# Performance work log

Measured on AMD Instinct MI355X. Metric: run time of the kernel, lower is better.

The kernel has to match this reference:

```python
import jax, jax.numpy as jnp
import numpy as np

B, T, C = 2, 4096, 768
H = 12
D = C // H  # head_size = 64


def setup_inputs() -> dict:
    key = jax.random.key(0)
    k1, k2, k3 = jax.random.split(key, 3)
    x = jax.random.normal(k1, (B, T, C), dtype=jnp.float32)
    w_attn = jax.random.normal(k2, (C, 3 * C), dtype=jnp.float32) * (C ** -0.5)
    b_attn = jnp.zeros((3 * C,), dtype=jnp.float32)
    w_proj = jax.random.normal(k3, (C, C), dtype=jnp.float32) * (C ** -0.5)
    b_proj = jnp.zeros((C,), dtype=jnp.float32)
    return {"x": x, "w_attn": w_attn, "b_attn": b_attn, "w_proj": w_proj, "b_proj": b_proj}


def reference(x, w_attn, b_attn, w_proj, b_proj):
    Bx, Tx, Cx = x.shape
    # fused QKV projection
    qkv = x @ w_attn + b_attn  # (B, T, 3C)
    q, k, v = jnp.split(qkv, 3, axis=2)
    # (B, H, T, D)
    q = q.reshape(Bx, Tx, H, D).transpose(0, 2, 1, 3)
    k = k.reshape(Bx, Tx, H, D).transpose(0, 2, 1, 3)
    v = v.reshape(Bx, Tx, H, D).transpose(0, 2, 1, 3)
    scale = 1.0 / jnp.sqrt(jnp.asarray(D, dtype=x.dtype))
    scores = jnp.einsum('bhqd,bhkd->bhqk', q, k) * scale  # (B, H, T, T)
    causal = jnp.tril(jnp.ones((Tx, Tx), dtype=bool))
    scores = jnp.where(causal, scores, jnp.asarray(-jnp.inf, dtype=scores.dtype))
    attn = jax.nn.softmax(scores, axis=-1)
    y = jnp.einsum('bhqk,bhkd->bhqd', attn, v)  # (B, H, T, D)
    y = y.transpose(0, 2, 1, 3).reshape(Bx, Tx, Cx)
    return y @ w_proj + b_proj
```

## Files before the change

kernel.cpp:

```cpp
#include <hip/hip_runtime.h>
#include <stdint.h>

#define B_   2
#define T_   4096
#define C_   768
#define H_   12
#define D_   64
#define BH_  24
#define M_   8192
#define K_   768
#define N1_  2304

#define NEG_BIG (-1.0e30f)
#define QSCALE 0.18033688011112042f

typedef short bf16x8 __attribute__((ext_vector_type(8)));
typedef float f32x4  __attribute__((ext_vector_type(4)));
typedef float f32x16 __attribute__((ext_vector_type(16)));
typedef uint32_t u32x4 __attribute__((ext_vector_type(4)));
typedef int i32x2 __attribute__((ext_vector_type(2)));

typedef const __attribute__((address_space(1))) void* as1cv;
typedef __attribute__((address_space(3))) void*       as3v;

__device__ __forceinline__ void gload_lds16(const void* g, void* l) {
  __builtin_amdgcn_global_load_lds((as1cv)g, (as3v)l, 16, 0, 0);
}

__device__ __forceinline__ unsigned short f2bf(float f) {
  uint32_t x = __builtin_bit_cast(uint32_t, f);
  uint32_t r = (x + 0x7fffu + ((x >> 16) & 1u)) >> 16;
  return (unsigned short)r;
}

__device__ __forceinline__ unsigned short f2bf_hu(float f) {
  return (unsigned short)((__builtin_bit_cast(uint32_t, f) + 0x8000u) >> 16);
}

#if __has_builtin(__builtin_amdgcn_perm)
__device__ __forceinline__ uint32_t pack_hu(float lo, float hi) {
  uint32_t a = __builtin_bit_cast(uint32_t, lo) + 0x8000u;
  uint32_t b = __builtin_bit_cast(uint32_t, hi) + 0x8000u;
  return __builtin_amdgcn_perm(b, a, 0x07060302u);
}
#else
__device__ __forceinline__ uint32_t pack_hu(float lo, float hi) {
  uint32_t a = __builtin_bit_cast(uint32_t, lo) + 0x8000u;
  uint32_t b = __builtin_bit_cast(uint32_t, hi) + 0x8000u;
  return (b & 0xFFFF0000u) | (a >> 16);
}
#endif

__device__ __forceinline__ float bfu(uint32_t w, int hb) {
  return __builtin_bit_cast(float, hb ? (w & 0xFFFF0000u) : (w << 16));
}

#if __has_builtin(__builtin_amdgcn_permlane32_swap)
#define HAVE_PLSWAP 1
#else
#define HAVE_PLSWAP 0
#endif

#if __has_builtin(__builtin_amdgcn_exp2f)
__device__ __forceinline__ float fast_exp2(float x) { return __builtin_amdgcn_exp2f(x); }
#else
__device__ __forceinline__ float fast_exp2(float x) { return __expf(x * 0.69314718056f); }
#endif

__global__ void cast_kernel(const float* __restrict__ in, unsigned short* __restrict__ out, int n4) {
  int idx = blockIdx.x * blockDim.x + threadIdx.x;
  int stride = gridDim.x * blockDim.x;
  for (int i = idx; i < n4; i += stride) {
    float4 v = reinterpret_cast<const float4*>(in)[i];
    ushort4 o;
    o.x = f2bf(v.x); o.y = f2bf(v.y); o.z = f2bf(v.z); o.w = f2bf(v.w);
    reinterpret_cast<ushort4*>(out)[i] = o;
  }
}

__global__ void transpose_cast2(const float* __restrict__ a, unsigned short* __restrict__ oa,
                                const float* __restrict__ b, unsigned short* __restrict__ ob) {
  __shared__ float tile[32][33];
  const int bx = blockIdx.x;
  const float* in; unsigned short* out; int N, cb;
  if (bx < 72) { in = a; out = oa; N = 2304; cb = bx; }
  else         { in = b; out = ob; N = 768;  cb = bx - 72; }
  const int tx = threadIdx.x, ty = threadIdx.y;
  const int n = cb * 32 + tx;
  #pragma unroll
  for (int r = 0; r < 4; ++r) {
    int k = blockIdx.y * 32 + ty + r * 8;
    tile[ty + r * 8][tx] = in[(size_t)k * N + n];
  }
  __syncthreads();
  const int k = blockIdx.y * 32 + tx;
  #pragma unroll
  for (int r = 0; r < 4; ++r) {
    int nn = cb * 32 + ty + r * 8;
    out[(size_t)nn * K_ + k] = f2bf(tile[tx][ty + r * 8]);
  }
}

template <int MODE>
__global__ __launch_bounds__(256) void gemm_kernel(
    const unsigned short* __restrict__ A, const unsigned short* __restrict__ BT,
    const float* __restrict__ bias,
    unsigned short* __restrict__ o0, unsigned short* __restrict__ o1,
    unsigned short* __restrict__ o2, float* __restrict__ fo) {
  __shared__ __align__(16) unsigned short Al[128 * 32];
  __shared__ __align__(16) unsigned short Bl[128 * 32];
  const int tid = threadIdx.x;
  const int w = tid >> 6, lane = tid & 63;
  const int g = lane >> 4, c16 = lane & 15;
  const int wr = w >> 1, wc = w & 1;
  const int m0 = blockIdx.x * 128, n0 = blockIdx.y * 128;

  f32x4 acc[4][4] = {};

  for (int k0 = 0; k0 < K_; k0 += 32) {
    __syncthreads();
    #pragma unroll
    for (int q = 0; q < 2; ++q) {
      const int ch = (w * 2 + q) * 64 + lane;
      const int row = ch >> 2, kb = ch & 3;
      gload_lds16(A  + (size_t)(m0 + row) * K_ + k0 + kb * 8, &Al[(w * 2 + q) * 512]);
      gload_lds16(BT + (size_t)(n0 + row) * K_ + k0 + kb * 8, &Bl[(w * 2 + q) * 512]);
    }
    __syncthreads();
    bf16x8 af[4], bfr[4];
    #pragma unroll
    for (int i = 0; i < 4; ++i) {
      af[i]  = *reinterpret_cast<const bf16x8*>(&Al[(wr * 64 + i * 16 + c16) * 32 + g * 8]);
      bfr[i] = *reinterpret_cast<const bf16x8*>(&Bl[(wc * 64 + i * 16 + c16) * 32 + g * 8]);
    }
    #pragma unroll
    for (int i = 0; i < 4; ++i)
      #pragma unroll
      for (int j = 0; j < 4; ++j)
        acc[i][j] = __builtin_amdgcn_mfma_f32_16x16x32_bf16(af[i], bfr[j], acc[i][j], 0, 0, 0);
  }

  const int which = (MODE == 0) ? (n0 / 768) : 0;
  #pragma unroll
  for (int i = 0; i < 4; ++i) {
    const int mbase = m0 + wr * 64 + i * 16 + g * 4;
    const int bb2 = mbase >> 12, tb = mbase & 4095;
    #pragma unroll
    for (int j2 = 0; j2 < 4; ++j2) {
      const int n = n0 + wc * 64 + j2 * 16 + c16;
      const float bv = bias[n];
      if constexpr (MODE == 0) {
        const int cc = n - which * 768;
        const int hh2 = cc >> 6, dd = cc & 63;
        const size_t hb = ((size_t)bb2 * H_ + hh2) * T_ * D_;
        if (which == 0) {
          const int addr0 = tb * 64 + dd;
          #pragma unroll
          for (int j = 0; j < 4; ++j)
            o0[hb + addr0 + j * 64] = f2bf_hu((acc[i][j2][j] + bv) * QSCALE);
        } else if (which == 1) {
          const int addr0 = ((tb >> 5) * 4 + (dd >> 4)) * 512 +
                            ((tb & 31) + ((dd >> 3) & 1) * 32) * 8 + (dd & 7);
          #pragma unroll
          for (int j = 0; j < 4; ++j)
            o1[hb + addr0 + j * 8] = f2bf_hu(acc[i][j2][j] + bv);
        } else {
          const int addr0 = (tb >> 6) * 4096 + (dd >> 5) * 2048 +
                            ((tb >> 4) & 3) * 512 +
                            ((dd & 31) + ((tb >> 3) & 1) * 32) * 8 + (tb & 7);
          #pragma unroll
          for (int j = 0; j < 4; ++j)
            o2[hb + addr0 + j] = f2bf_hu(acc[i][j2][j] + bv);
        }
      } else {
        #pragma unroll
        for (int j = 0; j < 4; ++j)
          fo[(size_t)(mbase + j) * 768 + n] = acc[i][j2][j] + bv;
      }
    }
  }
}

__global__ __launch_bounds__(256, 2) void attn_kernel(
    const unsigned short* __restrict__ Qb, const unsigned short* __restrict__ Kb,
    const unsigned short* __restrict__ Vt, unsigned short* __restrict__ Yb) {
  __shared__ float Ml[3][2][64];
  __shared__ float Ll[3][2][64];
  __shared__ uint32_t Ylp[3][32][64];

  const int tidx = threadIdx.x;
  const int wv = tidx >> 6;
  const int lane = tidx & 63;
  const int q31 = lane & 31, hi = lane >> 5;
  const int bid = blockIdx.x;
  const int bh = bid % BH_;
  const int strip = (T_ / 64 - 1) - bid / BH_;
  const int q0 = strip * 64;
  const int qgA = q0 + q31;
  const int qgB = q0 + 32 + q31;

  const int bb = bh / H_, hh = bh % H_;
  const size_t hoff = (size_t)bh * T_ * D_;
  const unsigned short* Qh = Qb + hoff;
  const unsigned short* Kh = Kb + hoff + lane * 8;
  const unsigned short* Vh = Vt + hoff + lane * 8;

  bf16x8 qfA[4], qfB[4];
  #pragma unroll
  for (int s = 0; s < 4; ++s) {
    qfA[s] = *reinterpret_cast<const bf16x8*>(&Qh[(size_t)qgA * D_ + s * 16 + hi * 8]);
    qfB[s] = *reinterpret_cast<const bf16x8*>(&Qh[(size_t)qgB * D_ + s * 16 + hi * 8]);
  }

  float mA = NEG_BIG, lA = 0.f, mB = NEG_BIG, lB = 0.f;
  f32x16 yA0 = {}, yA1 = {}, yB0 = {}, yB1 = {};

  const int nt = strip + 1;

  bf16x8 kf[8];
  {
    const unsigned short* kT = Kh + wv * 4096;
    #pragma unroll
    for (int s = 0; s < 8; ++s)
      kf[s] = *reinterpret_cast<const bf16x8*>(kT + (s >> 2) * 2048 + (s & 3) * 512);
  }

  for (int it = wv; it < nt; it += 4) {
    const int kv0 = it << 6;

    const unsigned short* vT = Vh + it * 4096;
    bf16x8 vlo[4], vhi[4];
    #pragma unroll
    for (int ks = 0; ks < 4; ++ks) {
      vlo[ks] = *reinterpret_cast<const bf16x8*>(vT + ks * 512);
      vhi[ks] = *reinterpret_cast<const bf16x8*>(vT + 2048 + ks * 512);
    }

    f32x16 sA0 = {}, sA1 = {}, sB0 = {}, sB1 = {};
    #pragma unroll
    for (int s = 0; s < 4; ++s) {
      sA0 = __builtin_amdgcn_mfma_f32_32x32x16_bf16(kf[s], qfA[s], sA0, 0, 0, 0);
      sB0 = __builtin_amdgcn_mfma_f32_32x32x16_bf16(kf[s], qfB[s], sB0, 0, 0, 0);
    }
    #pragma unroll
    for (int s = 0; s < 4; ++s) {
      sA1 = __builtin_amdgcn_mfma_f32_32x32x16_bf16(kf[4 + s], qfA[s], sA1, 0, 0, 0);
      sB1 = __builtin_amdgcn_mfma_f32_32x32x16_bf16(kf[4 + s], qfB[s], sB1, 0, 0, 0);
    }

    {
      const unsigned short* kT = Kh + (it + 4) * 4096;
      #pragma unroll
      for (int s = 0; s < 8; ++s)
        kf[s] = *reinterpret_cast<const bf16x8*>(kT + (s >> 2) * 2048 + (s & 3) * 512);
    }

    if (it == strip) {
      #pragma unroll
      for (int r = 0; r < 16; ++r) {
        const int kvl = (r & 3) + 8 * (r >> 2) + 4 * hi;
        sA0[r] = (kv0 + kvl > qgA)      ? NEG_BIG : sA0[r];
        sA1[r] = NEG_BIG;
        sB1[r] = (kv0 + 32 + kvl > qgB) ? NEG_BIG : sB1[r];
      }
    }

    {
      float a[16];
      #pragma unroll
      for (int r = 0; r < 8; ++r) a[r] = fmaxf(sA0[2 * r], sA0[2 * r + 1]);
      #pragma unroll
      for (int r = 0; r < 8; ++r) a[8 + r] = fmaxf(sA1[2 * r], sA1[2 * r + 1]);
      #pragma unroll
      for (int st = 8; st > 0; st >>= 1)
        #pragma unroll
        for (int r = 0; r < 16; ++r) if (r < st) a[r] = fmaxf(a[r], a[r + st]);
      float tmax = a[0];
      tmax = fmaxf(tmax, __shfl_xor(tmax, 32));

      if (__any(tmax > mA + 11.5f)) {
        const float mnew = fmaxf(mA, tmax);
        const float alpha = fast_exp2(mA - mnew);
        mA = mnew;
        lA *= alpha;
        #pragma unroll
        for (int r = 0; r < 16; ++r) { yA0[r] *= alpha; yA1[r] *= alpha; }
      }
      #pragma unroll
      for (int r = 0; r < 16; ++r) {
        sA0[r] = fast_exp2(sA0[r] - mA);
        sA1[r] = fast_exp2(sA1[r] - mA);
      }
      #pragma unroll
      for (int r = 0; r < 8; ++r) a[r] = sA0[2 * r] + sA0[2 * r + 1];
      #pragma unroll
      for (int r = 0; r < 8; ++r) a[8 + r] = sA1[2 * r] + sA1[2 * r + 1];
      #pragma unroll
      for (int st = 8; st > 0; st >>= 1)
        #pragma unroll
        for (int r = 0; r < 16; ++r) if (r < st) a[r] = a[r] + a[r + st];
      float rsum = a[0];
      rsum += __shfl_xor(rsum, 32);
      lA += rsum;

      bf16x8 pf[4];
#if HAVE_PLSWAP
#define MK_PF(KS, SH, GA, HA)                                                 \
      {                                                                       \
        uint32_t g0 = pack_hu(SH[(GA)*4 + 0], SH[(GA)*4 + 1]);                \
        uint32_t g1 = pack_hu(SH[(GA)*4 + 2], SH[(GA)*4 + 3]);                \
        uint32_t h0 = pack_hu(SH[(HA)*4 + 0], SH[(HA)*4 + 1]);                \
        uint32_t h1 = pack_hu(SH[(HA)*4 + 2], SH[(HA)*4 + 3]);                \
        i32x2 r0 = __builtin_amdgcn_permlane32_swap((int)g0, (int)h0, false, false); \
        i32x2 r1 = __builtin_amdgcn_permlane32_swap((int)g1, (int)h1, false, false); \
        u32x4 t;                                                              \
        t[0] = (uint32_t)r0[0];                                               \
        t[1] = (uint32_t)r1[0];                                               \
        t[2] = (uint32_t)r0[1];                                               \
        t[3] = (uint32_t)r1[1];                                               \
        pf[KS] = __builtin_bit_cast(bf16x8, t);                               \
      }
#else
#define MK_PF(KS, SH, GA, HA)                                                 \
      {                                                                       \
        uint32_t g0 = pack_hu(SH[(GA)*4 + 0], SH[(GA)*4 + 1]);                \
        uint32_t g1 = pack_hu(SH[(GA)*4 + 2], SH[(GA)*4 + 3]);                \
        uint32_t h0 = pack_hu(SH[(HA)*4 + 0], SH[(HA)*4 + 1]);                \
        uint32_t h1 = pack_hu(SH[(HA)*4 + 2], SH[(HA)*4 + 3]);                \
        uint32_t sg0 = (uint32_t)__shfl_xor((int)g0, 32);                     \
        uint32_t sg1 = (uint32_t)__shfl_xor((int)g1, 32);                     \
        uint32_t sh0 = (uint32_t)__shfl_xor((int)h0, 32);                     \
        uint32_t sh1 = (uint32_t)__shfl_xor((int)h1, 32);                     \
        u32x4 t;                                                              \
        t[0] = hi ? sh0 : g0;                                                 \
        t[1] = hi ? sh1 : g1;                                                 \
        t[2] = hi ? h0 : sg0;                                                 \
        t[3] = hi ? h1 : sg1;                                                 \
        pf[KS] = __builtin_bit_cast(bf16x8, t);                               \
      }
#endif
      MK_PF(0, sA0, 0, 1)
      MK_PF(1, sA0, 2, 3)
      MK_PF(2, sA1, 0, 1)
      MK_PF(3, sA1, 2, 3)

      #pragma unroll
      for (int ks = 0; ks < 4; ++ks)
        yA0 = __builtin_amdgcn_mfma_f32_32x32x16_bf16(vlo[ks], pf[ks], yA0, 0, 0, 0);
      #pragma unroll
      for (int ks = 0; ks < 4; ++ks)
        yA1 = __builtin_amdgcn_mfma_f32_32x32x16_bf16(vhi[ks], pf[ks], yA1, 0, 0, 0);
    }

    {
      float a[16];
      #pragma unroll
      for (int r = 0; r < 8; ++r) a[r] = fmaxf(sB0[2 * r], sB0[2 * r + 1]);
      #pragma unroll
      for (int r = 0; r < 8; ++r) a[8 + r] = fmaxf(sB1[2 * r], sB1[2 * r + 1]);
      #pragma unroll
      for (int st = 8; st > 0; st >>= 1)
        #pragma unroll
        for (int r = 0; r < 16; ++r) if (r < st) a[r] = fmaxf(a[r], a[r + st]);
      float tmax = a[0];
      tmax = fmaxf(tmax, __shfl_xor(tmax, 32));

      if (__any(tmax > mB + 11.5f)) {
        const float mnew = fmaxf(mB, tmax);
        const float alpha = fast_exp2(mB - mnew);
        mB = mnew;
        lB *= alpha;
        #pragma unroll
        for (int r = 0; r < 16; ++r) { yB0[r] *= alpha; yB1[r] *= alpha; }
      }
      #pragma unroll
      for (int r = 0; r < 16; ++r) {
        sB0[r] = fast_exp2(sB0[r] - mB);
        sB1[r] = fast_exp2(sB1[r] - mB);
      }
      #pragma unroll
      for (int r = 0; r < 8; ++r) a[r] = sB0[2 * r] + sB0[2 * r + 1];
      #pragma unroll
      for (int r = 0; r < 8; ++r) a[8 + r] = sB1[2 * r] + sB1[2 * r + 1];
      #pragma unroll
      for (int st = 8; st > 0; st >>= 1)
        #pragma unroll
        for (int r = 0; r < 16; ++r) if (r < st) a[r] = a[r] + a[r + st];
      float rsum = a[0];
      rsum += __shfl_xor(rsum, 32);
      lB += rsum;

      bf16x8 pf[4];
      MK_PF(0, sB0, 0, 1)
      MK_PF(1, sB0, 2, 3)
      MK_PF(2, sB1, 0, 1)
      MK_PF(3, sB1, 2, 3)
#undef MK_PF

      #pragma unroll
      for (int ks = 0; ks < 4; ++ks)
        yB0 = __builtin_amdgcn_mfma_f32_32x32x16_bf16(vlo[ks], pf[ks], yB0, 0, 0, 0);
      #pragma unroll
      for (int ks = 0; ks < 4; ++ks)
        yB1 = __builtin_amdgcn_mfma_f32_32x32x16_bf16(vhi[ks], pf[ks], yB1, 0, 0, 0);
    }
  }

  if (wv > 0) {
    Ml[wv - 1][0][lane] = mA; Ml[wv - 1][1][lane] = mB;
    Ll[wv - 1][0][lane] = lA; Ll[wv - 1][1][lane] = lB;
    #pragma unroll
    for (int r = 0; r < 8; ++r) {
      Ylp[wv - 1][r][lane]      = pack_hu(yA0[2 * r], yA0[2 * r + 1]);
      Ylp[wv - 1][8 + r][lane]  = pack_hu(yA1[2 * r], yA1[2 * r + 1]);
      Ylp[wv - 1][16 + r][lane] = pack_hu(yB0[2 * r], yB0[2 * r + 1]);
      Ylp[wv - 1][24 + r][lane] = pack_hu(yB1[2 * r], yB1[2 * r + 1]);
    }
  }
  __syncthreads();
  if (wv == 0) {
    {
      float mm = mA;
      #pragma unroll
      for (int p = 0; p < 3; ++p) mm = fmaxf(mm, Ml[p][0][lane]);
      const float aw = fast_exp2(mA - mm);
      float ap[3];
      float ll = lA * aw;
      #pragma unroll
      for (int p = 0; p < 3; ++p) {
        ap[p] = fast_exp2(Ml[p][0][lane] - mm);
        ll += Ll[p][0][lane] * ap[p];
      }
      const float inv = 1.f / ll;
      const size_t ro = ((size_t)bb * T_ + qgA) * C_ + hh * D_;
      #pragma unroll
      for (int q2 = 0; q2 < 4; ++q2) {
        float v[8];
        #pragma unroll
        for (int e = 0; e < 4; ++e) {
          const int pr = q2 * 2 + (e >> 1), hb2 = e & 1;
          float t0 = yA0[q2 * 4 + e] * aw;
          float t1 = yA1[q2 * 4 + e] * aw;
          #pragma unroll
          for (int p = 0; p < 3; ++p) {
            t0 += bfu(Ylp[p][pr][lane], hb2) * ap[p];
            t1 += bfu(Ylp[p][8 + pr][lane], hb2) * ap[p];
          }
          v[e] = t0 * inv;
          v[4 + e] = t1 * inv;
        }
        uint2 pr0 = {pack_hu(v[0], v[1]), pack_hu(v[2], v[3])};
        *reinterpret_cast<uint2*>(&Yb[ro + q2 * 8 + hi * 4]) = pr0;
        uint2 pr1 = {pack_hu(v[4], v[5]), pack_hu(v[6], v[7])};
        *reinterpret_cast<uint2*>(&Yb[ro + 32 + q2 * 8 + hi * 4]) = pr1;
      }
    }
    {
      float mm = mB;
      #pragma unroll
      for (int p = 0; p < 3; ++p) mm = fmaxf(mm, Ml[p][1][lane]);
      const float aw = fast_exp2(mB - mm);
      float ap[3];
      float ll = lB * aw;
      #pragma unroll
      for (int p = 0; p < 3; ++p) {
        ap[p] = fast_exp2(Ml[p][1][lane] - mm);
        ll += Ll[p][1][lane] * ap[p];
      }
      const float inv = 1.f / ll;
      const size_t ro = ((size_t)bb * T_ + qgB) * C_ + hh * D_;
      #pragma unroll
      for (int q2 = 0; q2 < 4; ++q2) {
        float v[8];
        #pragma unroll
        for (int e = 0; e < 4; ++e) {
          const int pr = q2 * 2 + (e >> 1), hb2 = e & 1;
          float t0 = yB0[q2 * 4 + e] * aw;
          float t1 = yB1[q2 * 4 + e] * aw;
          #pragma unroll
          for (int p = 0; p < 3; ++p) {
            t0 += bfu(Ylp[p][16 + pr][lane], hb2) * ap[p];
            t1 += bfu(Ylp[p][24 + pr][lane], hb2) * ap[p];
          }
          v[e] = t0 * inv;
          v[4 + e] = t1 * inv;
        }
        uint2 pr0 = {pack_hu(v[0], v[1]), pack_hu(v[2], v[3])};
        *reinterpret_cast<uint2*>(&Yb[ro + q2 * 8 + hi * 4]) = pr0;
        uint2 pr1 = {pack_hu(v[4], v[5]), pack_hu(v[6], v[7])};
        *reinterpret_cast<uint2*>(&Yb[ro + 32 + q2 * 8 + hi * 4]) = pr1;
      }
    }
  }
}

extern "C" void kernel_launch(void* const* d_in, const int* in_sizes, int n_in,
                              void* d_out, int out_size, void* d_ws, size_t ws_size,
                              hipStream_t stream) {
  const float* x      = (const float*)d_in[0];
  const float* w_attn = (const float*)d_in[1];
  const float* b_attn = (const float*)d_in[2];
  const float* w_proj = (const float*)d_in[3];
  const float* b_proj = (const float*)d_in[4];
  float* out = (float*)d_out;

  char* ws = (char*)d_ws;
  size_t off = 0;
  auto alloc = [&](size_t bytes) -> void* {
    void* p = ws + off;
    off += (bytes + 255) & ~(size_t)255;
    return p;
  };
  unsigned short* xb  = (unsigned short*)alloc((size_t)M_ * K_ * 2);
  unsigned short* waT = (unsigned short*)alloc((size_t)N1_ * K_ * 2);
  unsigned short* wpT = (unsigned short*)alloc((size_t)C_ * K_ * 2);
  unsigned short* Qb  = (unsigned short*)alloc((size_t)BH_ * T_ * D_ * 2);
  unsigned short* Kb  = (unsigned short*)alloc((size_t)BH_ * T_ * D_ * 2);
  unsigned short* Vt  = (unsigned short*)alloc((size_t)BH_ * D_ * T_ * 2);
  unsigned short* Yb  = (unsigned short*)alloc((size_t)M_ * C_ * 2);

  cast_kernel<<<1024, 256, 0, stream>>>(x, xb, M_ * K_ / 4);
  transpose_cast2<<<dim3(96, 24), dim3(32, 8), 0, stream>>>(w_attn, waT, w_proj, wpT);

  gemm_kernel<0><<<dim3(M_ / 128, N1_ / 128), 256, 0, stream>>>(
      xb, waT, b_attn, Qb, Kb, Vt, nullptr);

  attn_kernel<<<(T_ / 64) * BH_, 256, 0, stream>>>(Qb, Kb, Vt, Yb);

  gemm_kernel<1><<<dim3(M_ / 128, C_ / 128), 256, 0, stream>>>(
      Yb, wpT, b_proj, nullptr, nullptr, nullptr, out);
}
```

Baseline: 166.7 us.

## Pair complementary causal strips per attention block and use max3 column reduction

New measurement: 176.5 us. 1.06x slower.

```diff
diff --git a/kernel.cpp b/kernel.cpp
--- a/kernel.cpp
+++ b/kernel.cpp
@@ -53,6 +53,10 @@
 
 __device__ __forceinline__ float bfu(uint32_t w, int hb) {
   return __builtin_bit_cast(float, hb ? (w & 0xFFFF0000u) : (w << 16));
+}
+
+__device__ __forceinline__ float max3f(float a, float b, float c) {
+  return fmaxf(fmaxf(a, b), c);
 }
 
 #if __has_builtin(__builtin_amdgcn_permlane32_swap)
@@ -194,10 +198,7 @@
   const int q31 = lane & 31, hi = lane >> 5;
   const int bid = blockIdx.x;
   const int bh = bid % BH_;
-  const int strip = (T_ / 64 - 1) - bid / BH_;
-  const int q0 = strip * 64;
-  const int qgA = q0 + q31;
-  const int qgB = q0 + 32 + q31;
+  const int jj = bid / BH_;
 
   const int bb = bh / H_, hh = bh % H_;
   const size_t hoff = (size_t)bh * T_ * D_;
@@ -205,292 +206,308 @@
   const unsigned short* Kh = Kb + hoff + lane * 8;
   const unsigned short* Vh = Vt + hoff + lane * 8;
 
-  bf16x8 qfA[4], qfB[4];
-  #pragma unroll
-  for (int s = 0; s < 4; ++s) {
-    qfA[s] = *reinterpret_cast<const bf16x8*>(&Qh[(size_t)qgA * D_ + s * 16 + hi * 8]);
-    qfB[s] = *reinterpret_cast<const bf16x8*>(&Qh[(size_t)qgB * D_ + s * 16 + hi * 8]);
-  }
-
-  float mA = NEG_BIG, lA = 0.f, mB = NEG_BIG, lB = 0.f;
-  f32x16 yA0 = {}, yA1 = {}, yB0 = {}, yB1 = {};
-
-  const int nt = strip + 1;
-
-  bf16x8 kf[8];
-  {
-    const unsigned short* kT = Kh + wv * 4096;
-    #pragma unroll
-    for (int s = 0; s < 8; ++s)
-      kf[s] = *reinterpret_cast<const bf16x8*>(kT + (s >> 2) * 2048 + (s & 3) * 512);
-  }
-
-  for (int it = wv; it < nt; it += 4) {
-    const int kv0 = it << 6;
-
-    const unsigned short* vT = Vh + it * 4096;
-    bf16x8 vlo[4], vhi[4];
-    #pragma unroll
-    for (int ks = 0; ks < 4; ++ks) {
-      vlo[ks] = *reinterpret_cast<const bf16x8*>(vT + ks * 512);
-      vhi[ks] = *reinterpret_cast<const bf16x8*>(vT + 2048 + ks * 512);
-    }
-
-    f32x16 sA0 = {}, sA1 = {}, sB0 = {}, sB1 = {};
+  const f32x16 vzero = {};
+
+  for (int sp = 0; sp < 2; ++sp) {
+    const int strip = sp ? jj : 63 - jj;
+    const int q0 = strip * 64;
+    const int qgA = q0 + q31;
+    const int qgB = q0 + 32 + q31;
+
+    bf16x8 qfA[4], qfB[4];
     #pragma unroll
     for (int s = 0; s < 4; ++s) {
-      sA0 = __builtin_amdgcn_mfma_f32_32x32x16_bf16(kf[s], qfA[s], sA0, 0, 0, 0);
-      sB0 = __builtin_amdgcn_mfma_f32_32x32x16_bf16(kf[s], qfB[s], sB0, 0, 0, 0);
-    }
-    #pragma unroll
-    for (int s = 0; s < 4; ++s) {
-      sA1 = __builtin_amdgcn_mfma_f32_32x32x16_bf16(kf[4 + s], qfA[s], sA1, 0, 0, 0);
-      sB1 = __builtin_amdgcn_mfma_f32_32x32x16_bf16(kf[4 + s], qfB[s], sB1, 0, 0, 0);
-    }
-
+      qfA[s] = *reinterpret_cast<const bf16x8*>(&Qh[(size_t)qgA * D_ + s * 16 + hi * 8]);
+      qfB[s] = *reinterpret_cast<const bf16x8*>(&Qh[(size_t)qgB * D_ + s * 16 + hi * 8]);
+    }
+
+    float mA = NEG_BIG, lA = 0.f, mB = NEG_BIG, lB = 0.f;
+    f32x16 yA0 = vzero, yA1 = vzero, yB0 = vzero, yB1 = vzero;
+
+    const int nt = strip + 1;
+
+    bf16x8 kf[8];
     {
-      const unsigned short* kT = Kh + (it + 4) * 4096;
+      const unsigned short* kT = Kh + wv * 4096;
       #pragma unroll
       for (int s = 0; s < 8; ++s)
         kf[s] = *reinterpret_cast<const bf16x8*>(kT + (s >> 2) * 2048 + (s & 3) * 512);
     }
 
-    if (it == strip) {
+    for (int it = wv; it < nt; it += 4) {
+      const int kv0 = it << 6;
+
+      const unsigned short* vT = Vh + it * 4096;
+      bf16x8 vlo[4], vhi[4];
       #pragma unroll
-      for (int r = 0; r < 16; ++r) {
-        const int kvl = (r & 3) + 8 * (r >> 2) + 4 * hi;
-        sA0[r] = (kv0 + kvl > qgA)      ? NEG_BIG : sA0[r];
-        sA1[r] = NEG_BIG;
-        sB1[r] = (kv0 + 32 + kvl > qgB) ? NEG_BIG : sB1[r];
-      }
-    }
-
-    {
-      float a[16];
+      for (int ks = 0; ks < 4; ++ks) {
+        vlo[ks] = *reinterpret_cast<const bf16x8*>(vT + ks * 512);
+        vhi[ks] = *reinterpret_cast<const bf16x8*>(vT + 2048 + ks * 512);
+      }
+
+      f32x16 sA0 = vzero, sA1 = vzero, sB0 = vzero, sB1 = vzero;
       #pragma unroll
-      for (int r = 0; r < 8; ++r) a[r] = fmaxf(sA0[2 * r], sA0[2 * r + 1]);
+      for (int s = 0; s < 4; ++s) {
+        sA0 = __builtin_amdgcn_mfma_f32_32x32x16_bf16(kf[s], qfA[s], sA0, 0, 0, 0);
+        sB0 = __builtin_amdgcn_mfma_f32_32x32x16_bf16(kf[s], qfB[s], sB0, 0, 0, 0);
+      }
       #pragma unroll
-      for (int r = 0; r < 8; ++r) a[8 + r] = fmaxf(sA1[2 * r], sA1[2 * r + 1]);
-      #pragma unroll
-      for (int st = 8; st > 0; st >>= 1)
-        #pragma unroll
-        for (int r = 0; r < 16; ++r) if (r < st) a[r] = fmaxf(a[r], a[r + st]);
-      float tmax = a[0];
-      tmax = fmaxf(tmax, __shfl_xor(tmax, 32));
-
-      if (__any(tmax > mA + 11.5f)) {
-        const float mnew = fmaxf(mA, tmax);
-        const float alpha = fast_exp2(mA - mnew);
-        mA = mnew;
-        lA *= alpha;
-        #pragma unroll
-        for (int r = 0; r < 16; ++r) { yA0[r] *= alpha; yA1[r] *= alpha; }
-      }
-      #pragma unroll
-      for (int r = 0; r < 16; ++r) {
-        sA0[r] = fast_exp2(sA0[r] - mA);
-        sA1[r] = fast_exp2(sA1[r] - mA);
-      }
-      #pragma unroll
-      for (int r = 0; r < 8; ++r) a[r] = sA0[2 * r] + sA0[2 * r + 1];
-      #pragma unroll
-      for (int r = 0; r < 8; ++r) a[8 + r] = sA1[2 * r] + sA1[2 * r + 1];
-      #pragma unroll
-      for (int st = 8; st > 0; st >>= 1)
-        #pragma unroll
-        for (int r = 0; r < 16; ++r) if (r < st) a[r] = a[r] + a[r + st];
-      float rsum = a[0];
-      rsum += __shfl_xor(rsum, 32);
-      lA += rsum;
-
-      bf16x8 pf[4];
+      for (int s = 0; s < 4; ++s) {
+        sA1 = __builtin_amdgcn_mfma_f32_32x32x16_bf16(kf[4 + s], qfA[s], sA1, 0, 0, 0);
+        sB1 = __builtin_amdgcn_mfma_f32_32x32x16_bf16(kf[4 + s], qfB[s], sB1, 0, 0, 0);
+      }
+
+      {
+        const unsigned short* kT = Kh + (it + 4) * 4096;
+        #pragma unroll
+        for (int s = 0; s < 8; ++s)
+          kf[s] = *reinterpret_cast<const bf16x8*>(kT + (s >> 2) * 2048 + (s & 3) * 512);
+      }
+
+      if (it == strip) {
+        #pragma unroll
+        for (int r = 0; r < 16; ++r) {
+          const int kvl = (r & 3) + 8 * (r >> 2) + 4 * hi;
+          sA0[r] = (kv0 + kvl > qgA)      ? NEG_BIG : sA0[r];
+          sA1[r] = NEG_BIG;
+          sB1[r] = (kv0 + 32 + kvl > qgB) ? NEG_BIG : sB1[r];
+        }
+      }
+
+#define COLMAX(S0, S1, TM)                                                    \
+      {                                                                       \
+        float g0 = max3f(S0[0], S0[1], S0[2]);                                \
+        float g1 = max3f(S0[3], S0[4], S0[5]);                                \
+        float g2 = max3f(S0[6], S0[7], S0[8]);                                \
+        float g3 = max3f(S0[9], S0[10], S0[11]);                              \
+        float g4 = max3f(S0[12], S0[13], S0[14]);                             \
+        float g5 = max3f(S0[15], S1[0], S1[1]);                               \
+        float g6 = max3f(S1[2], S1[3], S1[4]);                                \
+        float g7 = max3f(S1[5], S1[6], S1[7]);                                \
+        float g8 = max3f(S1[8], S1[9], S1[10]);                               \
+        float g9 = max3f(S1[11], S1[12], S1[13]);                             \
+        float ga = fmaxf(S1[14], S1[15]);                                     \
+        float h0 = max3f(g0, g1, g2);                                         \
+        float h1 = max3f(g3, g4, g5);                                         \
+        float h2 = max3f(g6, g7, g8);                                         \
+        float h3 = max3f(g9, ga, h0);                                         \
+        TM = max3f(h1, h2, h3);                                               \
+        TM = fmaxf(TM, __shfl_xor(TM, 32));                                   \
+      }
+
+      {
+        float tmax;
+        COLMAX(sA0, sA1, tmax)
+
+        if (__any(tmax > mA + 11.5f)) {
+          const float mnew = fmaxf(mA, tmax);
+          const float alpha = fast_exp2(mA - mnew);
+          mA = mnew;
+          lA *= alpha;
+          #pragma unroll
+          for (int r = 0; r < 16; ++r) { yA0[r] *= alpha; yA1[r] *= alpha; }
+        }
+        #pragma unroll
+        for (int r = 0; r < 16; ++r) {
+          sA0[r] = fast_exp2(sA0[r] - mA);
+          sA1[r] = fast_exp2(sA1[r] - mA);
+        }
+        float a[16];
+        #pragma unroll
+        for (int r = 0; r < 8; ++r) a[r] = sA0[2 * r] + sA0[2 * r + 1];
+        #pragma unroll
+        for (int r = 0; r < 8; ++r) a[8 + r] = sA1[2 * r] + sA1[2 * r + 1];
+        #pragma unroll
+        for (int st = 8; st > 0; st >>= 1)
+          #pragma unroll
+          for (int r = 0; r < 16; ++r) if (r < st) a[r] = a[r] + a[r + st];
+        float rsum = a[0];
+        rsum += __shfl_xor(rsum, 32);
+        lA += rsum;
+
+        bf16x8 pf[4];
 #if HAVE_PLSWAP
 #define MK_PF(KS, SH, GA, HA)                                                 \
-      {                                                                       \
-        uint32_t g0 = pack_hu(SH[(GA)*4 + 0], SH[(GA)*4 + 1]);                \
-        uint32_t g1 = pack_hu(SH[(GA)*4 + 2], SH[(GA)*4 + 3]);                \
-        uint32_t h0 = pack_hu(SH[(HA)*4 + 0], SH[(HA)*4 + 1]);                \
-        uint32_t h1 = pack_hu(SH[(HA)*4 + 2], SH[(HA)*4 + 3]);                \
-        i32x2 r0 = __builtin_amdgcn_permlane32_swap((int)g0, (int)h0, false, false); \
-        i32x2 r1 = __builtin_amdgcn_permlane32_swap((int)g1, (int)h1, false, false); \
-        u32x4 t;                                                              \
-        t[0] = (uint32_t)r0[0];                                               \
-        t[1] = (uint32_t)r1[0];                                               \
-        t[2] = (uint32_t)r0[1];                                               \
-        t[3] = (uint32_t)r1[1];                                               \
-        pf[KS] = __builtin_bit_cast(bf16x8, t);                               \
-      }
+        {                                                                     \
+          uint32_t g0 = pack_hu(SH[(GA)*4 + 0], SH[(GA)*4 + 1]);              \
+          uint32_t g1 = pack_hu(SH[(GA)*4 + 2], SH[(GA)*4 + 3]);              \
+          uint32_t h0 = pack_hu(SH[(HA)*4 + 0], SH[(HA)*4 + 1]);              \
+          uint32_t h1 = pack_hu(SH[(HA)*4 + 2], SH[(HA)*4 + 3]);              \
+          i32x2 r0 = __builtin_amdgcn_permlane32_swap((int)g0, (int)h0, false, false); \
+          i32x2 r1 = __builtin_amdgcn_permlane32_swap((int)g1, (int)h1, false, false); \
+          u32x4 t;                                                            \
+          t[0] = (uint32_t)r0[0];                                             \
+          t[1] = (uint32_t)r1[0];                                             \
+          t[2] = (uint32_t)r0[1];                                             \
+          t[3] = (uint32_t)r1[1];                                             \
+          pf[KS] = __builtin_bit_cast(bf16x8, t);                             \
+        }
 #else
 #define MK_PF(KS, SH, GA, HA)                                                 \
-      {                                                                       \
-        uint32_t g0 = pack_hu(SH[(GA)*4 + 0], SH[(GA)*4 + 1]);                \
-        uint32_t g1 = pack_hu(SH[(GA)*4 + 2], SH[(GA)*4 + 3]);                \
-        uint32_t h0 = pack_hu(SH[(HA)*4 + 0], SH[(HA)*4 + 1]);                \
-        uint32_t h1 = pack_hu(SH[(HA)*4 + 2], SH[(HA)*4 + 3]);                \
-        uint32_t sg0 = (uint32_t)__shfl_xor((int)g0, 32);                     \
-        uint32_t sg1 = (uint32_t)__shfl_xor((int)g1, 32);                     \
-        uint32_t sh0 = (uint32_t)__shfl_xor((int)h0, 32);                     \
-        uint32_t sh1 = (uint32_t)__shfl_xor((int)h1, 32);                     \
-        u32x4 t;                                                              \
-        t[0] = hi ? sh0 : g0;                                                 \
-        t[1] = hi ? sh1 : g1;                                                 \
-        t[2] = hi ? h0 : sg0;                                                 \
-        t[3] = hi ? h1 : sg1;                                                 \
-        pf[KS] = __builtin_bit_cast(bf16x8, t);                               \
-      }
+        {                                                                     \
+          uint32_t g0 = pack_hu(SH[(GA)*4 + 0], SH[(GA)*4 + 1]);              \
+          uint32_t g1 = pack_hu(SH[(GA)*4 + 2], SH[(GA)*4 + 3]);              \
+          uint32_t h0 = pack_hu(SH[(HA)*4 + 0], SH[(HA)*4 + 1]);              \
+          uint32_t h1 = pack_hu(SH[(HA)*4 + 2], SH[(HA)*4 + 3]);              \
+          uint32_t sg0 = (uint32_t)__shfl_xor((int)g0, 32);                   \
+          uint32_t sg1 = (uint32_t)__shfl_xor((int)g1, 32);                   \
+          uint32_t sh0 = (uint32_t)__shfl_xor((int)h0, 32);                   \
+          uint32_t sh1 = (uint32_t)__shfl_xor((int)h1, 32);                   \
+          u32x4 t;                                                            \
+          t[0] = hi ? sh0 : g0;                                               \
+          t[1] = hi ? sh1 : g1;                                               \
+          t[2] = hi ? h0 : sg0;                                               \
+          t[3] = hi ? h1 : sg1;                                               \
+          pf[KS] = __builtin_bit_cast(bf16x8, t);                             \
+        }
 #endif
-      MK_PF(0, sA0, 0, 1)
-      MK_PF(1, sA0, 2, 3)
-      MK_PF(2, sA1, 0, 1)
-      MK_PF(3, sA1, 2, 3)
-
+        MK_PF(0, sA0, 0, 1)
+        MK_PF(1, sA0, 2, 3)
+        MK_PF(2, sA1, 0, 1)
+        MK_PF(3, sA1, 2, 3)
+
+        #pragma unroll
+        for (int ks = 0; ks < 4; ++ks)
+          yA0 = __builtin_amdgcn_mfma_f32_32x32x16_bf16(vlo[ks], pf[ks], yA0, 0, 0, 0);
+        #pragma unroll
+        for (int ks = 0; ks < 4; ++ks)
+          yA1 = __builtin_amdgcn_mfma_f32_32x32x16_bf16(vhi[ks], pf[ks], yA1, 0, 0, 0);
+      }
+
+      {
+        float tmax;
+        COLMAX(sB0, sB1, tmax)
+
+        if (__any(tmax > mB + 11.5f)) {
+          const float mnew = fmaxf(mB, tmax);
+          const float alpha = fast_exp2(mB - mnew);
+          mB = mnew;
+          lB *= alpha;
+          #pragma unroll
+          for (int r = 0; r < 16; ++r) { yB0[r] *= alpha; yB1[r] *= alpha; }
+        }
+        #pragma unroll
+        for (int r = 0; r < 16; ++r) {
+          sB0[r] = fast_exp2(sB0[r] - mB);
+          sB1[r] = fast_exp2(sB1[r] - mB);
+        }
+        float a[16];
+        #pragma unroll
+        for (int r = 0; r < 8; ++r) a[r] = sB0[2 * r] + sB0[2 * r + 1];
+        #pragma unroll
+        for (int r = 0; r < 8; ++r) a[8 + r] = sB1[2 * r] + sB1[2 * r + 1];
+        #pragma unroll
+        for (int st = 8; st > 0; st >>= 1)
+          #pragma unroll
+          for (int r = 0; r < 16; ++r) if (r < st) a[r] = a[r] + a[r + st];
+        float rsum = a[0];
+        rsum += __shfl_xor(rsum, 32);
+        lB += rsum;
+
+        bf16x8 pf[4];
+        MK_PF(0, sB0, 0, 1)
+        MK_PF(1, sB0, 2, 3)
+        MK_PF(2, sB1, 0, 1)
+        MK_PF(3, sB1, 2, 3)
+#undef MK_PF
+#undef COLMAX
+
+        #pragma unroll
+        for (int ks = 0; ks < 4; ++ks)
+          yB0 = __builtin_amdgcn_mfma_f32_32x32x16_bf16(vlo[ks], pf[ks], yB0, 0, 0, 0);
+        #pragma unroll
+        for (int ks = 0; ks < 4; ++ks)
+          yB1 = __builtin_amdgcn_mfma_f32_32x32x16_bf16(vhi[ks], pf[ks], yB1, 0, 0, 0);
+      }
+    }
+
+    if (wv > 0) {
+      Ml[wv - 1][0][lane] = mA; Ml[wv - 1][1][lane] = mB;
+      Ll[wv - 1][0][lane] = lA; Ll[wv - 1][1][lane] = lB;
       #pragma unroll
-      for (int ks = 0; ks < 4; ++ks)
-        yA0 = __builtin_amdgcn_mfma_f32_32x32x16_bf16(vlo[ks], pf[ks], yA0, 0, 0, 0);
-      #pragma unroll
-      for (int ks = 0; ks < 4; ++ks)
-        yA1 = __builtin_amdgcn_mfma_f32_32x32x16_bf16(vhi[ks], pf[ks], yA1, 0, 0, 0);
-    }
-
-    {
-      float a[16];
-      #pragma unroll
-      for (int r = 0; r < 8; ++r) a[r] = fmaxf(sB0[2 * r], sB0[2 * r + 1]);
-      #pragma unroll
-      for (int r = 0; r < 8; ++r) a[8 + r] = fmaxf(sB1[2 * r], sB1[2 * r + 1]);
-      #pragma unroll
-      for (int st = 8; st > 0; st >>= 1)
-        #pragma unroll
-        for (int r = 0; r < 16; ++r) if (r < st) a[r] = fmaxf(a[r], a[r + st]);
-      float tmax = a[0];
-      tmax = fmaxf(tmax, __shfl_xor(tmax, 32));
-
-      if (__any(tmax > mB + 11.5f)) {
-        const float mnew = fmaxf(mB, tmax);
-        const float alpha = fast_exp2(mB - mnew);
-        mB = mnew;
-        lB *= alpha;
-        #pragma unroll
-        for (int r = 0; r < 16; ++r) { yB0[r] *= alpha; yB1[r] *= alpha; }
-      }
-      #pragma unroll
-      for (int r = 0; r < 16; ++r) {
-        sB0[r] = fast_exp2(sB0[r] - mB);
-        sB1[r] = fast_exp2(sB1[r] - mB);
-      }
-      #pragma unroll
-      for (int r = 0; r < 8; ++r) a[r] = sB0[2 * r] + sB0[2 * r + 1];
-      #pragma unroll
-      for (int r = 0; r < 8; ++r) a[8 + r] = sB1[2 * r] + sB1[2 * r + 1];
-      #pragma unroll
-      for (int st = 8; st > 0; st >>= 1)
-        #pragma unroll
-        for (int r = 0; r < 16; ++r) if (r < st) a[r] = a[r] + a[r + st];
-      float rsum = a[0];
-      rsum += __shfl_xor(rsum, 32);
-      lB += rsum;
-
-      bf16x8 pf[4];
-      MK_PF(0, sB0, 0, 1)
-      MK_PF(1, sB0, 2, 3)
-      MK_PF(2, sB1, 0, 1)
-      MK_PF(3, sB1, 2, 3)
-#undef MK_PF
-
-      #pragma unroll
-      for (int ks = 0; ks < 4; ++ks)
-        yB0 = __builtin_amdgcn_mfma_f32_32x32x16_bf16(vlo[ks], pf[ks], yB0, 0, 0, 0);
-      #pragma unroll
-      for (int ks = 0; ks < 4; ++ks)
-        yB1 = __builtin_amdgcn_mfma_f32_32x32x16_bf16(vhi[ks], pf[ks], yB1, 0, 0, 0);
-    }
-  }
-
-  if (wv > 0) {
-    Ml[wv - 1][0][lane] = mA; Ml[wv - 1][1][lane] = mB;
-    Ll[wv - 1][0][lane] = lA; Ll[wv - 1][1][lane] = lB;
-    #pragma unroll
-    for (int r = 0; r < 8; ++r) {
-      Ylp[wv - 1][r][lane]      = pack_hu(yA0[2 * r], yA0[2 * r + 1]);
-      Ylp[wv - 1][8 + r][lane]  = pack_hu(yA1[2 * r], yA1[2 * r + 1]);
-      Ylp[wv - 1][16 + r][lane] = pack_hu(yB0[2 * r], yB0[2 * r + 1]);
-      Ylp[wv - 1][24 + r][lane] = pack_hu(yB1[2 * r], yB1[2 * r + 1]);
-    }
-  }
-  __syncthreads();
-  if (wv == 0) {
-    {
-      float mm = mA;
-      #pragma unroll
-      for (int p = 0; p < 3; ++p) mm = fmaxf(mm, Ml[p][0][lane]);
-      const float aw = fast_exp2(mA - mm);
-      float ap[3];
-      float ll = lA * aw;
-      #pragma unroll
-      for (int p = 0; p < 3; ++p) {
-        ap[p] = fast_exp2(Ml[p][0][lane] - mm);
-        ll += Ll[p][0][lane] * ap[p];
-      }
-      const float inv = 1.f / ll;
-      const size_t ro = ((size_t)bb * T_ + qgA) * C_ + hh * D_;
-      #pragma unroll
-      for (int q2 = 0; q2 < 4; ++q2) {
-        float v[8];
-        #pragma unroll
-        for (int e = 0; e < 4; ++e) {
-          const int pr = q2 * 2 + (e >> 1), hb2 = e & 1;
-          float t0 = yA0[q2 * 4 + e] * aw;
-          float t1 = yA1[q2 * 4 + e] * aw;
-          #pragma unroll
-          for (int p = 0; p < 3; ++p) {
-            t0 += bfu(Ylp[p][pr][lane], hb2) * ap[p];
-            t1 += bfu(Ylp[p][8 + pr][lane], hb2) * ap[p];
+      for (int r = 0; r < 8; ++r) {
+        Ylp[wv - 1][r][lane]      = pack_hu(yA0[2 * r], yA0[2 * r + 1]);
+        Ylp[wv - 1][8 + r][lane]  = pack_hu(yA1[2 * r], yA1[2 * r + 1]);
+        Ylp[wv - 1][16 + r][lane] = pack_hu(yB0[2 * r], yB0[2 * r + 1]);
+        Ylp[wv - 1][24 + r][lane] = pack_hu(yB1[2 * r], yB1[2 * r + 1]);
+      }
+    }
+    __syncthreads();
+    if (wv == 0) {
+      {
+        float mm = mA;
+        #pragma unroll
+        for (int p = 0; p < 3; ++p) mm = fmaxf(mm, Ml[p][0][lane]);
+        const float aw = fast_exp2(mA - mm);
+        float ap[3];
+        float ll = lA * aw;
+        #pragma unroll
+        for (int p = 0; p < 3; ++p) {
+          ap[p] = fast_exp2(Ml[p][0][lane] - mm);
+          ll += Ll[p][0][lane] * ap[p];
+        }
+        const float inv = 1.f / ll;
+        const size_t ro = ((size_t)bb * T_ + qgA) * C_ + hh * D_;
+        #pragma unroll
+        for (int q2 = 0; q2 < 4; ++q2) {
+          float v[8];
+          #pragma unroll
+          for (int e = 0; e < 4; ++e) {
+            const int pr = q2 * 2 + (e >> 1), hb2 = e & 1;
+            float t0 = yA0[q2 * 4 + e] * aw;
+            float t1 = yA1[q2 * 4 + e] * aw;
+            #pragma unroll
+            for (int p = 0; p < 3; ++p) {
+              t0 += bfu(Ylp[p][pr][lane], hb2) * ap[p];
+              t1 += bfu(Ylp[p][8 + pr][lane], hb2) * ap[p];
+            }
+            v[e] = t0 * inv;
+            v[4 + e] = t1 * inv;
           }
-          v[e] = t0 * inv;
-          v[4 + e] = t1 * inv;
-        }
-        uint2 pr0 = {pack_hu(v[0], v[1]), pack_hu(v[2], v[3])};
-        *reinterpret_cast<uint2*>(&Yb[ro + q2 * 8 + hi * 4]) = pr0;
-        uint2 pr1 = {pack_hu(v[4], v[5]), pack_hu(v[6], v[7])};
-        *reinterpret_cast<uint2*>(&Yb[ro + 32 + q2 * 8 + hi * 4]) = pr1;
-      }
-    }
-    {
-      float mm = mB;
-      #pragma unroll
-      for (int p = 0; p < 3; ++p) mm = fmaxf(mm, Ml[p][1][lane]);
-      const float aw = fast_exp2(mB - mm);
-      float ap[3];
-      float ll = lB * aw;
-      #pragma unroll
-      for (int p = 0; p < 3; ++p) {
-        ap[p] = fast_exp2(Ml[p][1][lane] - mm);
-        ll += Ll[p][1][lane] * ap[p];
-      }
-      const float inv = 1.f / ll;
-      const size_t ro = ((size_t)bb * T_ + qgB) * C_ + hh * D_;
-      #pragma unroll
-      for (int q2 = 0; q2 < 4; ++q2) {
-        float v[8];
-        #pragma unroll
-        for (int e = 0; e < 4; ++e) {
-          const int pr = q2 * 2 + (e >> 1), hb2 = e & 1;
-          float t0 = yB0[q2 * 4 + e] * aw;
-          float t1 = yB1[q2 * 4 + e] * aw;
-          #pragma unroll
-          for (int p = 0; p < 3; ++p) {
-            t0 += bfu(Ylp[p][16 + pr][lane], hb2) * ap[p];
-            t1 += bfu(Ylp[p][24 + pr][lane], hb2) * ap[p];
+          uint2 pr0 = {pack_hu(v[0], v[1]), pack_hu(v[2], v[3])};
+          *reinterpret_cast<uint2*>(&Yb[ro + q2 * 8 + hi * 4]) = pr0;
+          uint2 pr1 = {pack_hu(v[4], v[5]), pack_hu(v[6], v[7])};
+          *reinterpret_cast<uint2*>(&Yb[ro + 32 + q2 * 8 + hi * 4]) = pr1;
+        }
+      }
+      {
+        float mm = mB;
+        #pragma unroll
+        for (int p = 0; p < 3; ++p) mm = fmaxf(mm, Ml[p][1][lane]);
+        const float aw = fast_exp2(mB - mm);
+        float ap[3];
+        float ll = lB * aw;
+        #pragma unroll
+        for (int p = 0; p < 3; ++p) {
+          ap[p] = fast_exp2(Ml[p][1][lane] - mm);
+          ll += Ll[p][1][lane] * ap[p];
+        }
+        const float inv = 1.f / ll;
+        const size_t ro = ((size_t)bb * T_ + qgB) * C_ + hh * D_;
+        #pragma unroll
+        for (int q2 = 0; q2 < 4; ++q2) {
+          float v[8];
+          #pragma unroll
+          for (int e = 0; e < 4; ++e) {
+            const int pr = q2 * 2 + (e >> 1), hb2 = e & 1;
+            float t0 = yB0[q2 * 4 + e] * aw;
+            float t1 = yB1[q2 * 4 + e] * aw;
+            #pragma unroll
+            for (int p = 0; p < 3; ++p) {
+              t0 += bfu(Ylp[p][16 + pr][lane], hb2) * ap[p];
+              t1 += bfu(Ylp[p][24 + pr][lane], hb2) * ap[p];
+            }
+            v[e] = t0 * inv;
+            v[4 + e] = t1 * inv;
           }
-          v[e] = t0 * inv;
-          v[4 + e] = t1 * inv;
-        }
-        uint2 pr0 = {pack_hu(v[0], v[1]), pack_hu(v[2], v[3])};
-        *reinterpret_cast<uint2*>(&Yb[ro + q2 * 8 + hi * 4]) = pr0;
-        uint2 pr1 = {pack_hu(v[4], v[5]), pack_hu(v[6], v[7])};
-        *reinterpret_cast<uint2*>(&Yb[ro + 32 + q2 * 8 + hi * 4]) = pr1;
-      }
-    }
+          uint2 pr0 = {pack_hu(v[0], v[1]), pack_hu(v[2], v[3])};
+          *reinterpret_cast<uint2*>(&Yb[ro + q2 * 8 + hi * 4]) = pr0;
+          uint2 pr1 = {pack_hu(v[4], v[5]), pack_hu(v[6], v[7])};
+          *reinterpret_cast<uint2*>(&Yb[ro + 32 + q2 * 8 + hi * 4]) = pr1;
+        }
+      }
+    }
+    if (sp == 0) __syncthreads();
   }
 }
 
@@ -525,7 +542,7 @@
   gemm_kernel<0><<<dim3(M_ / 128, N1_ / 128), 256, 0, stream>>>(
       xb, waT, b_attn, Qb, Kb, Vt, nullptr);
 
-  attn_kernel<<<(T_ / 64) * BH_, 256, 0, stream>>>(Qb, Kb, Vt, Yb);
+  attn_kernel<<<32 * BH_, 256, 0, stream>>>(Qb, Kb, Vt, Yb);
 
   gemm_kernel<1><<<dim3(M_ / 128, C_ / 128), 256, 0, stream>>>(
       Yb, wpT, b_proj, nullptr, nullptr, nullptr, out);
```
